# Optimization experiments

Measured on AMD Instinct MI355X. Metric: run time of the kernel, lower is better.

Reference implementation:

```python
import jax, jax.numpy as jnp
import numpy as np

KEYS = 11     # inference_keys: number of heatmap channels / keypoints
NSTACK = 4
B, H, W = 16, 128, 128


def setup_inputs() -> dict:
    key = jax.random.key(0)
    k1, k2, k3 = jax.random.split(key, 3)
    combined_preds = jax.random.normal(k1, (B, NSTACK, 2 * KEYS, H, W), dtype=jnp.float32)
    heatmaps = jax.random.uniform(k2, (B, KEYS, H, W), dtype=jnp.float32)
    # labels[..., 9] and [..., 10] are keypoint coords; scale to [0, 160) so some
    # fall outside [0, H)=[0,128) and exercise the validity-mask branch.
    labels = jax.random.uniform(k3, (B, KEYS, 11), dtype=jnp.float32) * 160.0
    return {"combined_preds": combined_preds, "heatmaps": heatmaps, "labels": labels}


def reference(combined_preds, heatmaps, labels):
    keys = KEYS
    hm = combined_preds[:, :, :keys]          # [B, S, K, H, W] heatmap preds
    lb = combined_preds[:, :, keys:]          # [B, S, K, H, W] label preds
    b, s, k, m, n = hm.shape                  # m = H, n = W (code uses m for both // and %)

    # HeatmapLoss per stack, vectorized over the stack dim
    heat_loss = ((hm - heatmaps[:, None]) ** 2).sum(axis=(2, 3, 4))  # [B, S]

    # LabelLoss, fully vectorized over (B, S, K)
    flat = hm.reshape(b, s, k, m * n)
    index = jnp.argmax(flat, axis=-1)         # [B, S, K]
    x = index // m                            # matches int(index / m) in original
    y = index % m
    # a[x, y] where a is the [H, W] heatmap -> flat[x * W + y]
    a_xy = jnp.take_along_axis(flat, (x * n + y)[..., None], axis=-1)[..., 0]

    pred = lb.reshape(b, s, k, -1)            # [B, S, K, H*W]
    lab = labels[:, None]                     # [B, 1, K, 11] broadcast over stacks

    gx, gy = lab[..., 9], lab[..., 10]
    valid = (gx > 0) & (gy > 0) & (gx < m) & (gy < n)

    xf = x.astype(pred.dtype)
    yf = y.astype(pred.dtype)
    xy_loss = (gx + lab[..., 7] - xf - pred[..., 7]) ** 2 \
            + (gy + lab[..., 8] - yf - pred[..., 8]) ** 2
    conf_loss = (1.0 - a_xy) ** 2
    class_loss = ((pred[..., 0:7] - lab[..., 0:7]) ** 2).sum(axis=-1)

    per_kp = jnp.where(valid, class_loss + xy_loss + conf_loss, 0.0)  # [B, S, K]
    label_loss = per_kp.sum(axis=-1)                                   # [B, S]

    return heat_loss, label_loss
```

## Files before the change

### kernel.cpp

```cpp
#include <hip/hip_runtime.h>
#include <math.h>

#define KEYS 11
#define NSTACK 4
#define NB 16
#define HH 128
#define WW 128
#define HW (HH * WW)

__global__ void kp_zero_out(float* out) {
    out[threadIdx.x] = 0.0f;
}

__global__ __launch_bounds__(256) void kp_loss_kernel(
    const float* __restrict__ cp,
    const float* __restrict__ heat,
    const float* __restrict__ lab,
    float* __restrict__ out)
{
    const int bid = blockIdx.x;
    const int k  = bid % KEYS;
    const int bs = bid / KEYS;
    const int s  = bs % NSTACK;
    const int b  = bs / NSTACK;

    const float* __restrict__ hm = cp + ((size_t)((b * NSTACK + s) * (2 * KEYS) + k)) * HW;
    const float* __restrict__ ht = heat + ((size_t)(b * KEYS + k)) * HW;

    const int tid = threadIdx.x;
    float sum  = 0.0f;
    float vmax = -INFINITY;
    int   imax = 0;

    const float4* __restrict__ hm4 = (const float4*)hm;
    const float4* __restrict__ ht4 = (const float4*)ht;

    #pragma unroll 4
    for (int i = tid; i < HW / 4; i += 256) {
        float4 a = hm4[i];
        float4 c = ht4[i];
        float d0 = a.x - c.x, d1 = a.y - c.y, d2 = a.z - c.z, d3 = a.w - c.w;
        sum += d0 * d0 + d1 * d1 + d2 * d2 + d3 * d3;
        int base = i * 4;
        if (a.x > vmax) { vmax = a.x; imax = base;     }
        if (a.y > vmax) { vmax = a.y; imax = base + 1; }
        if (a.z > vmax) { vmax = a.z; imax = base + 2; }
        if (a.w > vmax) { vmax = a.w; imax = base + 3; }
    }

    #pragma unroll
    for (int off = 32; off > 0; off >>= 1) {
        float ov = __shfl_down(vmax, off);
        int   oi = __shfl_down(imax, off);
        float os = __shfl_down(sum,  off);
        sum += os;
        if (ov > vmax || (ov == vmax && oi < imax)) { vmax = ov; imax = oi; }
    }

    __shared__ float s_sum[4];
    __shared__ float s_v[4];
    __shared__ int   s_i[4];
    const int wave = tid >> 6;
    if ((tid & 63) == 0) { s_sum[wave] = sum; s_v[wave] = vmax; s_i[wave] = imax; }
    __syncthreads();

    if (tid == 0) {
        #pragma unroll
        for (int w = 1; w < 4; w++) {
            sum += s_sum[w];
            if (s_v[w] > vmax || (s_v[w] == vmax && s_i[w] < imax)) {
                vmax = s_v[w]; imax = s_i[w];
            }
        }
        atomicAdd(&out[bs], sum);

        const float* __restrict__ lb = cp + ((size_t)((b * NSTACK + s) * (2 * KEYS) + KEYS + k)) * HW;
        const float* __restrict__ L  = lab + (size_t)(b * KEYS + k) * 11;
        float gx = L[9], gy = L[10];
        bool valid = (gx > 0.0f) && (gy > 0.0f) && (gx < (float)HH) && (gy < (float)WW);
        if (valid) {
            float xf = (float)(imax / WW);
            float yf = (float)(imax % WW);
            float dx = gx + L[7] - xf - lb[7];
            float dy = gy + L[8] - yf - lb[8];
            float loss = dx * dx + dy * dy;
            float cm = 1.0f - vmax;
            loss += cm * cm;
            #pragma unroll
            for (int j = 0; j < 7; j++) {
                float d = lb[j] - L[j];
                loss += d * d;
            }
            atomicAdd(&out[64 + bs], loss);
        }
    }
}

extern "C" void kernel_launch(void* const* d_in, const int* in_sizes, int n_in,
                              void* d_out, int out_size, void* d_ws, size_t ws_size,
                              hipStream_t stream) {
    const float* cp   = (const float*)d_in[0];
    const float* heat = (const float*)d_in[1];
    const float* lab  = (const float*)d_in[2];
    float* out = (float*)d_out;

    kp_zero_out<<<1, 128, 0, stream>>>(out);
    kp_loss_kernel<<<NB * NSTACK * KEYS, 256, 0, stream>>>(cp, heat, lab, out);
}
```

Baseline: 136.1 us.

## Process all stacks per block to reuse target heatmap loads and drop atomics

Each block now handles one (batch, key) pair across all four stacks, so the target heatmap is read once instead of four times, and the loads use nontemporal hints. Atomics and the zeroing kernel are replaced by per-block partials written to a workspace and summed by a small final kernel, which also gives a deterministic result. In exchange the grid shrinks from 704 to 176 blocks, which may leave many compute units idle on a large GPU. Register pressure also rises with four accumulators per thread.

```diff
diff --git a/kernel.cpp b/kernel.cpp
--- a/kernel.cpp
+++ b/kernel.cpp
@@ -8,92 +8,124 @@
 #define WW 128
 #define HW (HH * WW)
 
-__global__ void kp_zero_out(float* out) {
-    out[threadIdx.x] = 0.0f;
-}
+typedef float f4 __attribute__((ext_vector_type(4)));
 
-__global__ __launch_bounds__(256) void kp_loss_kernel(
+__global__ __launch_bounds__(256) void kp_main(
     const float* __restrict__ cp,
     const float* __restrict__ heat,
     const float* __restrict__ lab,
-    float* __restrict__ out)
+    float* __restrict__ ws)
 {
-    const int bid = blockIdx.x;
-    const int k  = bid % KEYS;
-    const int bs = bid / KEYS;
-    const int s  = bs % NSTACK;
-    const int b  = bs / NSTACK;
+    const int grp = blockIdx.x;
+    const int b = grp / KEYS;
+    const int k = grp % KEYS;
+    const int tid = threadIdx.x;
 
-    const float* __restrict__ hm = cp + ((size_t)((b * NSTACK + s) * (2 * KEYS) + k)) * HW;
-    const float* __restrict__ ht = heat + ((size_t)(b * KEYS + k)) * HW;
+    const f4* __restrict__ ht4 = (const f4*)(heat + (size_t)grp * HW);
+    const f4* __restrict__ hm0 = (const f4*)(cp + ((size_t)((b * NSTACK + 0) * (2 * KEYS) + k)) * HW);
+    const f4* __restrict__ hm1 = (const f4*)(cp + ((size_t)((b * NSTACK + 1) * (2 * KEYS) + k)) * HW);
+    const f4* __restrict__ hm2 = (const f4*)(cp + ((size_t)((b * NSTACK + 2) * (2 * KEYS) + k)) * HW);
+    const f4* __restrict__ hm3 = (const f4*)(cp + ((size_t)((b * NSTACK + 3) * (2 * KEYS) + k)) * HW);
 
-    const int tid = threadIdx.x;
-    float sum  = 0.0f;
-    float vmax = -INFINITY;
-    int   imax = 0;
-
-    const float4* __restrict__ hm4 = (const float4*)hm;
-    const float4* __restrict__ ht4 = (const float4*)ht;
+    float sum[NSTACK]  = {0.0f, 0.0f, 0.0f, 0.0f};
+    float vmax[NSTACK] = {-INFINITY, -INFINITY, -INFINITY, -INFINITY};
+    int   imax[NSTACK] = {0, 0, 0, 0};
 
     #pragma unroll 4
     for (int i = tid; i < HW / 4; i += 256) {
-        float4 a = hm4[i];
-        float4 c = ht4[i];
-        float d0 = a.x - c.x, d1 = a.y - c.y, d2 = a.z - c.z, d3 = a.w - c.w;
-        sum += d0 * d0 + d1 * d1 + d2 * d2 + d3 * d3;
-        int base = i * 4;
-        if (a.x > vmax) { vmax = a.x; imax = base;     }
-        if (a.y > vmax) { vmax = a.y; imax = base + 1; }
-        if (a.z > vmax) { vmax = a.z; imax = base + 2; }
-        if (a.w > vmax) { vmax = a.w; imax = base + 3; }
+        f4 c = __builtin_nontemporal_load(ht4 + i);
+        f4 a[NSTACK];
+        a[0] = __builtin_nontemporal_load(hm0 + i);
+        a[1] = __builtin_nontemporal_load(hm1 + i);
+        a[2] = __builtin_nontemporal_load(hm2 + i);
+        a[3] = __builtin_nontemporal_load(hm3 + i);
+        const int base = i * 4;
+        #pragma unroll
+        for (int s = 0; s < NSTACK; ++s) {
+            float d0 = a[s][0] - c[0], d1 = a[s][1] - c[1];
+            float d2 = a[s][2] - c[2], d3 = a[s][3] - c[3];
+            sum[s] += d0 * d0 + d1 * d1 + d2 * d2 + d3 * d3;
+            if (a[s][0] > vmax[s]) { vmax[s] = a[s][0]; imax[s] = base;     }
+            if (a[s][1] > vmax[s]) { vmax[s] = a[s][1]; imax[s] = base + 1; }
+            if (a[s][2] > vmax[s]) { vmax[s] = a[s][2]; imax[s] = base + 2; }
+            if (a[s][3] > vmax[s]) { vmax[s] = a[s][3]; imax[s] = base + 3; }
+        }
     }
 
     #pragma unroll
     for (int off = 32; off > 0; off >>= 1) {
-        float ov = __shfl_down(vmax, off);
-        int   oi = __shfl_down(imax, off);
-        float os = __shfl_down(sum,  off);
-        sum += os;
-        if (ov > vmax || (ov == vmax && oi < imax)) { vmax = ov; imax = oi; }
+        #pragma unroll
+        for (int s = 0; s < NSTACK; ++s) {
+            float ov = __shfl_down(vmax[s], off);
+            int   oi = __shfl_down(imax[s], off);
+            float os = __shfl_down(sum[s],  off);
+            sum[s] += os;
+            if (ov > vmax[s] || (ov == vmax[s] && oi < imax[s])) { vmax[s] = ov; imax[s] = oi; }
+        }
     }
 
-    __shared__ float s_sum[4];
-    __shared__ float s_v[4];
-    __shared__ int   s_i[4];
+    __shared__ float s_sum[4][NSTACK];
+    __shared__ float s_v[4][NSTACK];
+    __shared__ int   s_i[4][NSTACK];
     const int wave = tid >> 6;
-    if ((tid & 63) == 0) { s_sum[wave] = sum; s_v[wave] = vmax; s_i[wave] = imax; }
+    if ((tid & 63) == 0) {
+        #pragma unroll
+        for (int s = 0; s < NSTACK; ++s) {
+            s_sum[wave][s] = sum[s]; s_v[wave][s] = vmax[s]; s_i[wave][s] = imax[s];
+        }
+    }
     __syncthreads();
 
-    if (tid == 0) {
+    if (tid < NSTACK) {
+        const int s = tid;
+        float fsum = s_sum[0][s];
+        float fv   = s_v[0][s];
+        int   fi   = s_i[0][s];
         #pragma unroll
         for (int w = 1; w < 4; w++) {
-            sum += s_sum[w];
-            if (s_v[w] > vmax || (s_v[w] == vmax && s_i[w] < imax)) {
-                vmax = s_v[w]; imax = s_i[w];
+            fsum += s_sum[w][s];
+            if (s_v[w][s] > fv || (s_v[w][s] == fv && s_i[w][s] < fi)) {
+                fv = s_v[w][s]; fi = s_i[w][s];
             }
         }
-        atomicAdd(&out[bs], sum);
+        ws[grp * NSTACK + s] = fsum;
 
         const float* __restrict__ lb = cp + ((size_t)((b * NSTACK + s) * (2 * KEYS) + KEYS + k)) * HW;
-        const float* __restrict__ L  = lab + (size_t)(b * KEYS + k) * 11;
+        const float* __restrict__ L  = lab + (size_t)grp * 11;
         float gx = L[9], gy = L[10];
         bool valid = (gx > 0.0f) && (gy > 0.0f) && (gx < (float)HH) && (gy < (float)WW);
+        float loss = 0.0f;
         if (valid) {
-            float xf = (float)(imax / WW);
-            float yf = (float)(imax % WW);
+            float xf = (float)(fi / WW);
+            float yf = (float)(fi % WW);
             float dx = gx + L[7] - xf - lb[7];
             float dy = gy + L[8] - yf - lb[8];
-            float loss = dx * dx + dy * dy;
-            float cm = 1.0f - vmax;
+            loss = dx * dx + dy * dy;
+            float cm = 1.0f - fv;
             loss += cm * cm;
             #pragma unroll
             for (int j = 0; j < 7; j++) {
                 float d = lb[j] - L[j];
                 loss += d * d;
             }
-            atomicAdd(&out[64 + bs], loss);
         }
+        ws[NB * KEYS * NSTACK + grp * NSTACK + s] = loss;
     }
+}
+
+__global__ void kp_final(const float* __restrict__ ws, float* __restrict__ out) {
+    const int bs = threadIdx.x;
+    const int b = bs / NSTACK;
+    const int s = bs % NSTACK;
+    float h = 0.0f, l = 0.0f;
+    #pragma unroll
+    for (int k = 0; k < KEYS; ++k) {
+        const int g = b * KEYS + k;
+        h += ws[g * NSTACK + s];
+        l += ws[NB * KEYS * NSTACK + g * NSTACK + s];
+    }
+    out[bs] = h;
+    out[64 + bs] = l;
 }
 
 extern "C" void kernel_launch(void* const* d_in, const int* in_sizes, int n_in,
@@ -103,7 +135,8 @@
     const float* heat = (const float*)d_in[1];
     const float* lab  = (const float*)d_in[2];
     float* out = (float*)d_out;
+    float* ws  = (float*)d_ws;
 
-    kp_zero_out<<<1, 128, 0, stream>>>(out);
-    kp_loss_kernel<<<NB * NSTACK * KEYS, 256, 0, stream>>>(cp, heat, lab, out);
+    kp_main<<<NB * KEYS, 256, 0, stream>>>(cp, heat, lab, ws);
+    kp_final<<<1, 64, 0, stream>>>(ws, out);
 }
```

New measurement: 143.9 us. +5.7%, slower.
